# Optimization experiments

Hardware: AMD Instinct MI355X
Metric: run time of the kernel (lower is better)

Reference implementation:

```python
import jax, jax.numpy as jnp
import numpy as np

N = 4096
K = 8


def setup_inputs() -> dict:
    key = jax.random.key(0)
    kA, kb, ka, kZ, kC = jax.random.split(key, 5)
    A = (jax.random.uniform(kA, (N, N)) < 0.01).astype(jnp.float32)
    beta = jax.random.normal(kb, (N,), dtype=jnp.float32)
    a = jax.random.normal(ka, (1,), dtype=jnp.float32)
    Z = jax.random.normal(kZ, (K, N), dtype=jnp.float32)
    C = jax.random.normal(kC, (N, K), dtype=jnp.float32)
    return {"A": A, "beta": beta, "a": a, "Z": Z, "C": C}


def reference(A, beta, a, Z, C):
    # beta_ij = beta_i + beta_j  -> [N, N]
    beta2 = beta[:, None] + beta[None, :]
    Zs = jax.nn.softmax(Z, axis=0)          # [K, N], softmax over archetypes
    Cs = jax.nn.softmax(C, axis=0)          # [N, K], softmax over nodes
    # M = (Zs @ Cs @ Zs).T -> [N, K] latent positions
    M = (Zs @ (Cs @ Zs)).T
    # Pairwise euclidean distance with the original's +1e-6 shift inside the square.
    diff = M[:, None, :] - M[None, :, :] + 1e-6   # [N, N, K]
    z_dist = jnp.sqrt(jnp.sum(diff * diff, axis=-1))  # [N, N]
    theta = beta2 - a[0] * z_dist
    sp = jax.nn.softplus(theta)
    # Zero the diagonal (theta - diag(diagonal(theta)) zeroes diag entries).
    d = jnp.arange(N)
    theta_off = theta.at[d, d].set(0.0)
    sp_off = sp.at[d, d].set(0.0)
    LL = jnp.sum(theta_off * A) - jnp.sum(sp_off)
    return LL
```

## Files before the change

### kernel.cpp

```cpp
#include <hip/hip_runtime.h>

#define N 4096
#define K 8
#define RB 64
#define CB 256
#define RCH 16
#define NCH (RB / RCH)
#define NPB 16

__device__ __forceinline__ float fast_exp2(float x) { return __builtin_amdgcn_exp2f(x); }
__device__ __forceinline__ float fast_log2(float x) { return __builtin_amdgcn_logf(x); }
__device__ __forceinline__ float fast_sqrt(float x) { return __builtin_amdgcn_sqrtf(x); }

__device__ __forceinline__ void load_lds_16B(const float* g, float* l) {
    __builtin_amdgcn_global_load_lds((const __attribute__((address_space(1))) void*)g,
                                     (__attribute__((address_space(3))) void*)l,
                                     16, 0, 0);
}

__global__ __launch_bounds__(256) void prep_stats(
    const float* __restrict__ Z, const float* __restrict__ C,
    float* __restrict__ ZsT, float* __restrict__ Upart, float* __restrict__ out)
{
    const int t = threadIdx.x;
    const int n = blockIdx.x * 256 + t;
    const float L2E = 1.44269504f;

    __shared__ float zsL[256 * K];
    __shared__ float eL[256 * K];
    __shared__ float red[4][64];

    if (blockIdx.x == 0 && t == 0) out[0] = 0.f;

    float z[K];
#pragma unroll
    for (int k = 0; k < K; ++k) z[k] = Z[k * N + n];
    float zmax = z[0];
#pragma unroll
    for (int k = 1; k < K; ++k) zmax = fmaxf(zmax, z[k]);
    float zs[K];
    float zsum = 0.f;
#pragma unroll
    for (int k = 0; k < K; ++k) { zs[k] = fast_exp2((z[k] - zmax) * L2E); zsum += zs[k]; }
    const float inv = 1.f / zsum;
#pragma unroll
    for (int k = 0; k < K; ++k) zs[k] *= inv;

    float4* zst_p = (float4*)(ZsT + (size_t)n * K);
    zst_p[0] = make_float4(zs[0], zs[1], zs[2], zs[3]);
    zst_p[1] = make_float4(zs[4], zs[5], zs[6], zs[7]);

    const float4* c_p = (const float4*)(C + (size_t)n * K);
    const float4 c0 = c_p[0], c1 = c_p[1];
    float e[K];
    e[0] = fast_exp2(c0.x * L2E); e[1] = fast_exp2(c0.y * L2E);
    e[2] = fast_exp2(c0.z * L2E); e[3] = fast_exp2(c0.w * L2E);
    e[4] = fast_exp2(c1.x * L2E); e[5] = fast_exp2(c1.y * L2E);
    e[6] = fast_exp2(c1.z * L2E); e[7] = fast_exp2(c1.w * L2E);

#pragma unroll
    for (int k = 0; k < K; ++k) { zsL[t * K + k] = zs[k]; eL[t * K + k] = e[k]; }
    __syncthreads();

    const int cell = t & 63, q = t >> 6;
    const int a = cell >> 3, b = cell & 7;
    float s = 0.f;
    const int n0 = q * 64;
#pragma unroll 4
    for (int nn = 0; nn < 64; ++nn)
        s = fmaf(zsL[(n0 + nn) * K + a], eL[(n0 + nn) * K + b], s);
    red[q][cell] = s;
    __syncthreads();
    if (t < 64)
        Upart[blockIdx.x * 64 + t] = red[0][t] + red[1][t] + red[2][t] + red[3][t];
}

__global__ __launch_bounds__(256) void prep_M(
    const float* __restrict__ ZsT, const float* __restrict__ Upart,
    const float* __restrict__ A, const float* __restrict__ beta,
    const float* __restrict__ a_ptr, float* __restrict__ M, float* __restrict__ out)
{
    const int t = threadIdx.x;
    const int n = blockIdx.x * 256 + t;
    const float L2E = 1.44269504f;
    const float LN2 = 0.69314718f;

    __shared__ float UL[64];
    __shared__ float SinvL[8];
    if (t < 64) {
        float s = 0.f;
#pragma unroll
        for (int blk = 0; blk < NPB; ++blk) s += Upart[blk * 64 + t];
        UL[t] = s;
    }
    __syncthreads();
    if (t < 8) {
        float s = 0.f;
#pragma unroll
        for (int a = 0; a < 8; ++a) s += UL[a * 8 + t];
        SinvL[t] = 1.f / s;
    }
    __syncthreads();

    const float4* zst_p = (const float4*)(ZsT + (size_t)n * K);
    const float4 z0 = zst_p[0], z1 = zst_p[1];
    float w[K];
    w[0] = z0.x * SinvL[0]; w[1] = z0.y * SinvL[1]; w[2] = z0.z * SinvL[2]; w[3] = z0.w * SinvL[3];
    w[4] = z1.x * SinvL[4]; w[5] = z1.y * SinvL[5]; w[6] = z1.z * SinvL[6]; w[7] = z1.w * SinvL[7];
    float m[K];
#pragma unroll
    for (int k = 0; k < K; ++k) {
        float acc = 0.f;
#pragma unroll
        for (int kk = 0; kk < K; ++kk) acc = fmaf(UL[k * K + kk], w[kk], acc);
        m[k] = acc;
    }
    float4* m_p = (float4*)(M + (size_t)n * K);
    m_p[0] = make_float4(m[0], m[1], m[2], m[3]);
    m_p[1] = make_float4(m[4], m[5], m[6], m[7]);

    const float av = A[(size_t)n * N + n];
    const float theta = fmaf(-a_ptr[0], 2.8284271247e-6f, 2.f * beta[n]);
    const float ex = fast_exp2(theta * L2E);
    const float sp = LN2 * fast_log2(1.f + ex);
    float d = fmaf(theta, av, -sp);

    for (int off = 32; off > 0; off >>= 1) d += __shfl_down(d, off, 64);
    __shared__ float wsum[4];
    const int lane = t & 63, wid = t >> 6;
    if (lane == 0) wsum[wid] = d;
    __syncthreads();
    if (t == 0) atomicAdd(out, -(wsum[0] + wsum[1] + wsum[2] + wsum[3]));
}

__global__ __launch_bounds__(256) void pair_ll(
    const float* __restrict__ A, const float* __restrict__ beta,
    const float* __restrict__ a_ptr, const float* __restrict__ M,
    float* __restrict__ out)
{
    const int t = threadIdx.x;
    const int lane = t & 63, w = t >> 6;
    const int i0 = blockIdx.x * RB;
    const int jbase = blockIdx.y * CB;
    const int j = jbase + t;
    const float L2E = 1.44269504f;
    const float LN2 = 0.69314718f;

    __shared__ __align__(16) float Abuf[2][RCH][CB];
    __shared__ __align__(16) float4 ntwoMi[RB][2];
    __shared__ __align__(8)  float2 rc[RB];
    __shared__ float wsum[4];

    if (t < RB) {
        const float4* mp = (const float4*)(M + (size_t)(i0 + t) * K);
        const float4 a0 = mp[0], a1 = mp[1];
        float v[K] = { a0.x + 1e-6f, a0.y + 1e-6f, a0.z + 1e-6f, a0.w + 1e-6f,
                       a1.x + 1e-6f, a1.y + 1e-6f, a1.z + 1e-6f, a1.w + 1e-6f };
        float s2 = 0.f;
#pragma unroll
        for (int k = 0; k < K; ++k) s2 = fmaf(v[k], v[k], s2);
        ntwoMi[t][0] = make_float4(-2.f * v[0], -2.f * v[1], -2.f * v[2], -2.f * v[3]);
        ntwoMi[t][1] = make_float4(-2.f * v[4], -2.f * v[5], -2.f * v[6], -2.f * v[7]);
        rc[t] = make_float2(s2, beta[i0 + t] * L2E);
    }

    const float4* mp = (const float4*)(M + (size_t)j * K);
    const float4 mj0 = mp[0], mj1 = mp[1];
    float mj2 = mj0.x * mj0.x;
    mj2 = fmaf(mj0.y, mj0.y, mj2); mj2 = fmaf(mj0.z, mj0.z, mj2);
    mj2 = fmaf(mj0.w, mj0.w, mj2); mj2 = fmaf(mj1.x, mj1.x, mj2);
    mj2 = fmaf(mj1.y, mj1.y, mj2); mj2 = fmaf(mj1.z, mj1.z, mj2);
    mj2 = fmaf(mj1.w, mj1.w, mj2);
    const float bjL2E = beta[j] * L2E;
    const float naL2E = -a_ptr[0] * L2E;

    {
        const float* g = A + (size_t)(i0 + w * 4) * N + jbase + lane * 4;
#pragma unroll
        for (int rr = 0; rr < 4; ++rr)
            load_lds_16B(g + (size_t)rr * N, &Abuf[0][w * 4 + rr][0]);
    }

    float acc_t = 0.f, acc_l = 0.f;
    int buf = 0;
    for (int c = 0; c < NCH; ++c) {
        __syncthreads();
        if (c + 1 < NCH) {
            const float* g = A + (size_t)(i0 + (c + 1) * RCH + w * 4) * N + jbase + lane * 4;
#pragma unroll
            for (int rr = 0; rr < 4; ++rr)
                load_lds_16B(g + (size_t)rr * N, &Abuf[buf ^ 1][w * 4 + rr][0]);
        }
#pragma unroll
        for (int r = 0; r < RCH; ++r) {
            const int ir = c * RCH + r;
            const float av = Abuf[buf][r][t];
            const float4 tm0 = ntwoMi[ir][0];
            const float4 tm1 = ntwoMi[ir][1];
            const float2 cc = rc[ir];
            float ss = cc.x + mj2;
            ss = fmaf(tm0.x, mj0.x, ss); ss = fmaf(tm0.y, mj0.y, ss);
            ss = fmaf(tm0.z, mj0.z, ss); ss = fmaf(tm0.w, mj0.w, ss);
            ss = fmaf(tm1.x, mj1.x, ss); ss = fmaf(tm1.y, mj1.y, ss);
            ss = fmaf(tm1.z, mj1.z, ss); ss = fmaf(tm1.w, mj1.w, ss);
            ss = fmaxf(ss, 0.f);
            const float dist = fast_sqrt(ss);
            const float t2 = fmaf(naL2E, dist, cc.y + bjL2E);
            const float ex = fast_exp2(t2);
            const float lp = fast_log2(1.f + ex);
            acc_t = fmaf(t2, av, acc_t);
            acc_l += lp;
        }
        buf ^= 1;
    }
    float acc = LN2 * (acc_t - acc_l);

    for (int off = 32; off > 0; off >>= 1) acc += __shfl_down(acc, off, 64);
    if (lane == 0) wsum[w] = acc;
    __syncthreads();
    if (t == 0) atomicAdd(out, wsum[0] + wsum[1] + wsum[2] + wsum[3]);
}

extern "C" void kernel_launch(void* const* d_in, const int* in_sizes, int n_in,
                              void* d_out, int out_size, void* d_ws, size_t ws_size,
                              hipStream_t stream)
{
    const float* A    = (const float*)d_in[0];
    const float* beta = (const float*)d_in[1];
    const float* a    = (const float*)d_in[2];
    const float* Z    = (const float*)d_in[3];
    const float* C    = (const float*)d_in[4];
    float* out = (float*)d_out;

    float* ws    = (float*)d_ws;
    float* ZsT   = ws;
    float* M     = ws + (size_t)N * K;
    float* Upart = ws + (size_t)2 * N * K;

    prep_stats<<<NPB, 256, 0, stream>>>(Z, C, ZsT, Upart, out);
    prep_M<<<NPB, 256, 0, stream>>>(ZsT, Upart, A, beta, a, M, out);

    dim3 grid(N / RB, N / CB);
    pair_ll<<<grid, 256, 0, stream>>>(A, beta, a, M, out);
}
```

Before: 114.2 us.

## Fold prep_M into prep_stats and pair_ll, recomputing latent positions per block

Removes the prep_M kernel. The diagonal term moves into prep_stats, and each pair_ll block now rebuilds the latent positions M for its rows and columns from ZsT and Upart instead of reading a stored M. The output is zeroed with a memset instead of inside the first kernel. This saves one kernel launch and the M round trip through memory. In exchange every one of the 1024 blocks redundantly reduces Upart and runs small 8x8 matvecs, and a memset node is added to the stream.

```diff
diff --git a/kernel.cpp b/kernel.cpp
--- a/kernel.cpp
+++ b/kernel.cpp
@@ -20,17 +20,23 @@
 
 __global__ __launch_bounds__(256) void prep_stats(
     const float* __restrict__ Z, const float* __restrict__ C,
+    const float* __restrict__ A, const float* __restrict__ beta,
+    const float* __restrict__ a_ptr,
     float* __restrict__ ZsT, float* __restrict__ Upart, float* __restrict__ out)
 {
     const int t = threadIdx.x;
     const int n = blockIdx.x * 256 + t;
     const float L2E = 1.44269504f;
+    const float LN2 = 0.69314718f;
 
     __shared__ float zsL[256 * K];
     __shared__ float eL[256 * K];
     __shared__ float red[4][64];
-
-    if (blockIdx.x == 0 && t == 0) out[0] = 0.f;
+    __shared__ float dsum[4];
+
+    const float av_diag = A[(size_t)n * N + n];
+    const float bn = beta[n];
+    const float a_v = a_ptr[0];
 
     float z[K];
 #pragma unroll
@@ -73,70 +79,22 @@
     __syncthreads();
     if (t < 64)
         Upart[blockIdx.x * 64 + t] = red[0][t] + red[1][t] + red[2][t] + red[3][t];
-}
-
-__global__ __launch_bounds__(256) void prep_M(
-    const float* __restrict__ ZsT, const float* __restrict__ Upart,
-    const float* __restrict__ A, const float* __restrict__ beta,
-    const float* __restrict__ a_ptr, float* __restrict__ M, float* __restrict__ out)
-{
-    const int t = threadIdx.x;
-    const int n = blockIdx.x * 256 + t;
-    const float L2E = 1.44269504f;
-    const float LN2 = 0.69314718f;
-
-    __shared__ float UL[64];
-    __shared__ float SinvL[8];
-    if (t < 64) {
-        float s = 0.f;
-#pragma unroll
-        for (int blk = 0; blk < NPB; ++blk) s += Upart[blk * 64 + t];
-        UL[t] = s;
-    }
-    __syncthreads();
-    if (t < 8) {
-        float s = 0.f;
-#pragma unroll
-        for (int a = 0; a < 8; ++a) s += UL[a * 8 + t];
-        SinvL[t] = 1.f / s;
-    }
-    __syncthreads();
-
-    const float4* zst_p = (const float4*)(ZsT + (size_t)n * K);
-    const float4 z0 = zst_p[0], z1 = zst_p[1];
-    float w[K];
-    w[0] = z0.x * SinvL[0]; w[1] = z0.y * SinvL[1]; w[2] = z0.z * SinvL[2]; w[3] = z0.w * SinvL[3];
-    w[4] = z1.x * SinvL[4]; w[5] = z1.y * SinvL[5]; w[6] = z1.z * SinvL[6]; w[7] = z1.w * SinvL[7];
-    float m[K];
-#pragma unroll
-    for (int k = 0; k < K; ++k) {
-        float acc = 0.f;
-#pragma unroll
-        for (int kk = 0; kk < K; ++kk) acc = fmaf(UL[k * K + kk], w[kk], acc);
-        m[k] = acc;
-    }
-    float4* m_p = (float4*)(M + (size_t)n * K);
-    m_p[0] = make_float4(m[0], m[1], m[2], m[3]);
-    m_p[1] = make_float4(m[4], m[5], m[6], m[7]);
-
-    const float av = A[(size_t)n * N + n];
-    const float theta = fmaf(-a_ptr[0], 2.8284271247e-6f, 2.f * beta[n]);
+
+    const float theta = fmaf(-a_v, 2.8284271247e-6f, 2.f * bn);
     const float ex = fast_exp2(theta * L2E);
     const float sp = LN2 * fast_log2(1.f + ex);
-    float d = fmaf(theta, av, -sp);
-
+    float d = fmaf(theta, av_diag, -sp);
     for (int off = 32; off > 0; off >>= 1) d += __shfl_down(d, off, 64);
-    __shared__ float wsum[4];
-    const int lane = t & 63, wid = t >> 6;
-    if (lane == 0) wsum[wid] = d;
-    __syncthreads();
-    if (t == 0) atomicAdd(out, -(wsum[0] + wsum[1] + wsum[2] + wsum[3]));
+    const int lane = t & 63, wd = t >> 6;
+    if (lane == 0) dsum[wd] = d;
+    __syncthreads();
+    if (t == 0) atomicAdd(out, -(dsum[0] + dsum[1] + dsum[2] + dsum[3]));
 }
 
 __global__ __launch_bounds__(256) void pair_ll(
     const float* __restrict__ A, const float* __restrict__ beta,
-    const float* __restrict__ a_ptr, const float* __restrict__ M,
-    float* __restrict__ out)
+    const float* __restrict__ a_ptr, const float* __restrict__ ZsT,
+    const float* __restrict__ Upart, float* __restrict__ out)
 {
     const int t = threadIdx.x;
     const int lane = t & 63, w = t >> 6;
@@ -149,13 +107,64 @@
     __shared__ __align__(16) float Abuf[2][RCH][CB];
     __shared__ __align__(16) float4 ntwoMi[RB][2];
     __shared__ __align__(8)  float2 rc[RB];
+    __shared__ float UL[64];
     __shared__ float wsum[4];
 
+    {
+        const float* g = A + (size_t)(i0 + w * 4) * N + jbase + lane * 4;
+#pragma unroll
+        for (int rr = 0; rr < 4; ++rr)
+            load_lds_16B(g + (size_t)rr * N, &Abuf[0][w * 4 + rr][0]);
+    }
+
+    if (t < 64) {
+        float s = 0.f;
+#pragma unroll
+        for (int blk = 0; blk < NPB; ++blk) s += Upart[blk * 64 + t];
+        UL[t] = s;
+    }
+    __syncthreads();
+
+    float sinv[8];
+#pragma unroll
+    for (int b = 0; b < 8; ++b) {
+        float s = 0.f;
+#pragma unroll
+        for (int a = 0; a < 8; ++a) s += UL[a * 8 + b];
+        sinv[b] = 1.f / s;
+    }
+
+    const float4* zp = (const float4*)(ZsT + (size_t)j * K);
+    const float4 z0 = zp[0], z1 = zp[1];
+    float wv[K] = { z0.x * sinv[0], z0.y * sinv[1], z0.z * sinv[2], z0.w * sinv[3],
+                    z1.x * sinv[4], z1.y * sinv[5], z1.z * sinv[6], z1.w * sinv[7] };
+    float mj[K];
+#pragma unroll
+    for (int k = 0; k < K; ++k) {
+        float acc = 0.f;
+#pragma unroll
+        for (int kk = 0; kk < K; ++kk) acc = fmaf(UL[k * K + kk], wv[kk], acc);
+        mj[k] = acc;
+    }
+    float mj2 = mj[0] * mj[0];
+#pragma unroll
+    for (int k = 1; k < K; ++k) mj2 = fmaf(mj[k], mj[k], mj2);
+    const float bjL2E = beta[j] * L2E;
+    const float naL2E = -a_ptr[0] * L2E;
+
     if (t < RB) {
-        const float4* mp = (const float4*)(M + (size_t)(i0 + t) * K);
-        const float4 a0 = mp[0], a1 = mp[1];
-        float v[K] = { a0.x + 1e-6f, a0.y + 1e-6f, a0.z + 1e-6f, a0.w + 1e-6f,
-                       a1.x + 1e-6f, a1.y + 1e-6f, a1.z + 1e-6f, a1.w + 1e-6f };
+        const float4* zp2 = (const float4*)(ZsT + (size_t)(i0 + t) * K);
+        const float4 y0 = zp2[0], y1 = zp2[1];
+        float wr[K] = { y0.x * sinv[0], y0.y * sinv[1], y0.z * sinv[2], y0.w * sinv[3],
+                        y1.x * sinv[4], y1.y * sinv[5], y1.z * sinv[6], y1.w * sinv[7] };
+        float v[K];
+#pragma unroll
+        for (int k = 0; k < K; ++k) {
+            float acc = 0.f;
+#pragma unroll
+            for (int kk = 0; kk < K; ++kk) acc = fmaf(UL[k * K + kk], wr[kk], acc);
+            v[k] = acc + 1e-6f;
+        }
         float s2 = 0.f;
 #pragma unroll
         for (int k = 0; k < K; ++k) s2 = fmaf(v[k], v[k], s2);
@@ -163,28 +172,11 @@
         ntwoMi[t][1] = make_float4(-2.f * v[4], -2.f * v[5], -2.f * v[6], -2.f * v[7]);
         rc[t] = make_float2(s2, beta[i0 + t] * L2E);
     }
-
-    const float4* mp = (const float4*)(M + (size_t)j * K);
-    const float4 mj0 = mp[0], mj1 = mp[1];
-    float mj2 = mj0.x * mj0.x;
-    mj2 = fmaf(mj0.y, mj0.y, mj2); mj2 = fmaf(mj0.z, mj0.z, mj2);
-    mj2 = fmaf(mj0.w, mj0.w, mj2); mj2 = fmaf(mj1.x, mj1.x, mj2);
-    mj2 = fmaf(mj1.y, mj1.y, mj2); mj2 = fmaf(mj1.z, mj1.z, mj2);
-    mj2 = fmaf(mj1.w, mj1.w, mj2);
-    const float bjL2E = beta[j] * L2E;
-    const float naL2E = -a_ptr[0] * L2E;
-
-    {
-        const float* g = A + (size_t)(i0 + w * 4) * N + jbase + lane * 4;
-#pragma unroll
-        for (int rr = 0; rr < 4; ++rr)
-            load_lds_16B(g + (size_t)rr * N, &Abuf[0][w * 4 + rr][0]);
-    }
+    __syncthreads();
 
     float acc_t = 0.f, acc_l = 0.f;
     int buf = 0;
     for (int c = 0; c < NCH; ++c) {
-        __syncthreads();
         if (c + 1 < NCH) {
             const float* g = A + (size_t)(i0 + (c + 1) * RCH + w * 4) * N + jbase + lane * 4;
 #pragma unroll
@@ -199,10 +191,10 @@
             const float4 tm1 = ntwoMi[ir][1];
             const float2 cc = rc[ir];
             float ss = cc.x + mj2;
-            ss = fmaf(tm0.x, mj0.x, ss); ss = fmaf(tm0.y, mj0.y, ss);
-            ss = fmaf(tm0.z, mj0.z, ss); ss = fmaf(tm0.w, mj0.w, ss);
-            ss = fmaf(tm1.x, mj1.x, ss); ss = fmaf(tm1.y, mj1.y, ss);
-            ss = fmaf(tm1.z, mj1.z, ss); ss = fmaf(tm1.w, mj1.w, ss);
+            ss = fmaf(tm0.x, mj[0], ss); ss = fmaf(tm0.y, mj[1], ss);
+            ss = fmaf(tm0.z, mj[2], ss); ss = fmaf(tm0.w, mj[3], ss);
+            ss = fmaf(tm1.x, mj[4], ss); ss = fmaf(tm1.y, mj[5], ss);
+            ss = fmaf(tm1.z, mj[6], ss); ss = fmaf(tm1.w, mj[7], ss);
             ss = fmaxf(ss, 0.f);
             const float dist = fast_sqrt(ss);
             const float t2 = fmaf(naL2E, dist, cc.y + bjL2E);
@@ -211,6 +203,7 @@
             acc_t = fmaf(t2, av, acc_t);
             acc_l += lp;
         }
+        if (c + 1 < NCH) __syncthreads();
         buf ^= 1;
     }
     float acc = LN2 * (acc_t - acc_l);
@@ -234,12 +227,11 @@
 
     float* ws    = (float*)d_ws;
     float* ZsT   = ws;
-    float* M     = ws + (size_t)N * K;
-    float* Upart = ws + (size_t)2 * N * K;
-
-    prep_stats<<<NPB, 256, 0, stream>>>(Z, C, ZsT, Upart, out);
-    prep_M<<<NPB, 256, 0, stream>>>(ZsT, Upart, A, beta, a, M, out);
+    float* Upart = ws + (size_t)N * K;
+
+    hipMemsetAsync(out, 0, sizeof(float), stream);
+    prep_stats<<<NPB, 256, 0, stream>>>(Z, C, A, beta, a, ZsT, Upart, out);
 
     dim3 grid(N / RB, N / CB);
-    pair_ll<<<grid, 256, 0, stream>>>(A, beta, a, M, out);
-}
+    pair_ll<<<grid, 256, 0, stream>>>(A, beta, a, ZsT, Upart, out);
+}
```

New measurement: 115.7 us. About the same (+1.3%).
